# Kernel tuning notes

Measured on AMD Instinct MI355X. Metric: run time of the kernel, lower is better.

Reference implementation:

```python
import jax, jax.numpy as jnp
import numpy as np

B, S, D, H, K = 8, 1024, 512, 512, 8  # batch, seq, input_dim, hidden, max neighbors


def setup_inputs() -> dict:
    key = jax.random.key(0)
    ks = jax.random.split(key, 10)
    p = lambda k, shape: (0.05 * jax.random.normal(k, shape, jnp.float32))
    return {
        "input_t": jax.random.normal(ks[0], (B, S, D), jnp.float32),
        "comb_idx": jax.random.randint(ks[1], (B, S, K), 0, S, jnp.int32),
        "comb_mask": jax.random.randint(ks[2], (B, S, K), 0, 2, jnp.int32),
        "order": jnp.arange(B, dtype=jnp.int64),
        # PyTorch LSTM params per direction; b = b_ih + b_hh fused (mathematically identical)
        "w_ih_f": p(ks[3], (4 * H, D)),
        "w_hh_f": p(ks[4], (4 * H, H)),
        "b_f": p(ks[5], (4 * H,)),
        "w_ih_b": p(ks[6], (4 * H, D)),
        "w_hh_b": p(ks[7], (4 * H, H)),
        "b_b": p(ks[8], (4 * H,)),
    }


def _lstm_scan(x_sbd, w_ih, w_hh, b, reverse):
    # x_sbd: [S, B, D]; PyTorch gate order i, f, g, o; zero initial state (inithidden)
    Bb = x_sbd.shape[1]
    Hh = w_hh.shape[1]
    h0 = jnp.zeros((Bb, Hh), x_sbd.dtype)
    c0 = jnp.zeros((Bb, Hh), x_sbd.dtype)

    def cell(carry, xt):
        h, c = carry
        z = xt @ w_ih.T + h @ w_hh.T + b
        i, f, g, o = jnp.split(z, 4, axis=-1)
        c = jax.nn.sigmoid(f) * c + jax.nn.sigmoid(i) * jnp.tanh(g)
        h = jax.nn.sigmoid(o) * jnp.tanh(c)
        return (h, c), h

    (hn, cn), hs = jax.lax.scan(cell, (h0, c0), x_sbd, reverse=reverse)
    return hs, hn, cn  # hs in original time order even when reverse=True


def reference(input_t, comb_idx, comb_mask, order, w_ih_f, w_hh_f, b_f, w_ih_b, w_hh_b, b_b):
    x = jnp.swapaxes(input_t, 0, 1)  # [S, B, D]
    hs_f, hn_f, cn_f = _lstm_scan(x, w_ih_f, w_hh_f, b_f, reverse=False)
    hs_b, hn_b, cn_b = _lstm_scan(x, w_ih_b, w_hh_b, b_b, reverse=True)
    padded = jnp.swapaxes(jnp.concatenate([hs_f, hs_b], axis=-1), 0, 1)  # [B, S, 2H]
    h_n = jnp.stack([hn_f, hn_b])  # [2, B, H]
    c_n = jnp.stack([cn_f, cn_b])

    # comb = batch_comb[order[idx]]
    ci = comb_idx[order]                                  # [B, S, K]
    cm = comb_mask[order].astype(padded.dtype)            # [B, S, K]
    gathered = jax.vmap(lambda xb, ib: xb[ib])(padded, ci)  # [B, S, K, 2H]
    neigh_sum = (gathered * cm[..., None]).sum(axis=2)    # [B, S, 2H]
    cnt = cm.sum(axis=-1)                                 # [B, S]
    rep = (padded + neigh_sum) / (1.0 + cnt)[..., None]   # (x_i + sum_j x_j) / (|comb_i| + 1)
    rep = rep[:, 1:-1, :]                                 # drop first/last token

    # reorder_batch_encoder_rep[order[i]] = rep[i]
    out = jnp.zeros_like(rep).at[order].set(rep)
    return out, h_n, c_n
```

## Files before the change

kernel.cpp:

```cpp
#include <hip/hip_runtime.h>
#include <stdint.h>

typedef unsigned short u16;
typedef unsigned long long u64;
typedef __attribute__((ext_vector_type(8))) short short8v;
typedef __attribute__((ext_vector_type(4))) float f32x4;

#define OUT_HN   8372224
#define OUT_CN   8380416

#define WS_FLAGS 0
#define WS_CSB   4096
#define WS_HSB0  36864
#define WS_HSB1  8433664
#define WS_ZX    16830464

__device__ __forceinline__ u16 f2bf(float f) {
  uint32_t u = __float_as_uint(f);
  u += 0x7FFFu + ((u >> 16) & 1u);
  return (u16)(u >> 16);
}
__device__ __forceinline__ float bf2f(u16 v) {
  return __uint_as_float(((uint32_t)v) << 16);
}
__device__ __forceinline__ short8v cvt8(const float* p) {
  float4 a = *(const float4*)p;
  float4 b = *(const float4*)(p + 4);
  short8v r;
  r[0] = (short)f2bf(a.x); r[1] = (short)f2bf(a.y);
  r[2] = (short)f2bf(a.z); r[3] = (short)f2bf(a.w);
  r[4] = (short)f2bf(b.x); r[5] = (short)f2bf(b.y);
  r[6] = (short)f2bf(b.z); r[7] = (short)f2bf(b.w);
  return r;
}

__global__ void k_init(uint32_t* flags) {
  if (threadIdx.x < 64) flags[threadIdx.x] = 0;
}

__global__ void k_zero(u16* h0, u16* h1, float* c) {
  int i = blockIdx.x * blockDim.x + threadIdx.x;
  if (i < 4096) { h0[i] = 0; h1[i] = 0; }
  if (i < 8192) c[i] = 0.f;
}

#define STAGE_X(tcol)                                                          \
  {                                                                            \
    _Pragma("unroll")                                                          \
    for (int half = 0; half < 2; ++half) {                                     \
      int g = tid + half * 256;                                                \
      int r = g >> 6, B = g & 63;                                              \
      const float* xr = xf + ((size_t)r * 1024 + (tcol)) * 512 + B * 8;        \
      float4 a = *(const float4*)xr;                                           \
      float4 b = *(const float4*)(xr + 4);                                     \
      short8v v;                                                               \
      v[0] = (short)f2bf(a.x); v[1] = (short)f2bf(a.y);                        \
      v[2] = (short)f2bf(a.z); v[3] = (short)f2bf(a.w);                        \
      v[4] = (short)f2bf(b.x); v[5] = (short)f2bf(b.y);                        \
      v[6] = (short)f2bf(b.z); v[7] = (short)f2bf(b.w);                        \
      *(short8v*)(xL + r * 512 + ((B ^ r) << 3)) = v;                          \
    }                                                                          \
  }

__global__ void k_zx(const float* __restrict__ xf,
                     const float* __restrict__ wihf, const float* __restrict__ wihb,
                     u16* __restrict__ zx, int s0, int seglen)
{
  const int nch  = seglen >> 5;
  const int bid  = blockIdx.x;
  const int chunk = bid % nch;
  const int wg   = (bid / nch) & 15;
  const int dir  = bid / (nch * 16);
  const int tid  = threadIdx.x;
  const int wid  = tid >> 6;
  const int lane = tid & 63;
  const int jbase = wg * 32;
  const float* wih = dir ? wihb : wihf;

  __shared__ u16 xL[8 * 512];
  __shared__ float zL[4 * 8 * 32];

  short8v bih[2][16];
  {
    const int rr = lane & 15;
    const int ko = (lane >> 4) * 8;
    #pragma unroll
    for (int nt = 0; nt < 2; ++nt) {
      const int row = wid * 512 + jbase + nt * 16 + rr;
      #pragma unroll
      for (int kt = 0; kt < 16; ++kt)
        bih[nt][kt] = cvt8(wih + (size_t)row * 512 + kt * 32 + ko);
    }
  }

  const int rB = lane & 7;
  const int q  = lane >> 4;
  const f32x4 fzero = {0.f, 0.f, 0.f, 0.f};

  for (int i = 0; i < 32; ++i) {
    const int sidx = chunk * 32 + i;
    const int gstep = s0 + sidx;
    const int tn = dir ? (1023 - gstep) : gstep;
    STAGE_X(tn);
    __syncthreads();
    f32x4 acc0 = fzero, acc1 = fzero;
    #pragma unroll
    for (int kt = 0; kt < 16; ++kt) {
      short8v ax = *(const short8v*)(xL + rB * 512 + (((kt * 4 + q) ^ rB) << 3));
      acc0 = __builtin_amdgcn_mfma_f32_16x16x32_bf16(ax, bih[0][kt], acc0, 0, 0, 0);
      acc1 = __builtin_amdgcn_mfma_f32_16x16x32_bf16(ax, bih[1][kt], acc1, 0, 0, 0);
    }
    if (lane < 32) {
      #pragma unroll
      for (int r = 0; r < 4; ++r) {
        const int brow = (lane >> 4) * 4 + r;
        zL[wid * 256 + brow * 32 + (lane & 15)]      = acc0[r];
        zL[wid * 256 + brow * 32 + 16 + (lane & 15)] = acc1[r];
      }
    }
    __syncthreads();
    if (tid < 128) {
      const int b = tid >> 4;
      const int r = (tid & 15) * 8;
      const int g = r >> 5;
      const int jj = r & 31;
      short8v v;
      #pragma unroll
      for (int w = 0; w < 8; ++w) v[w] = (short)f2bf(zL[g * 256 + b * 32 + jj + w]);
      *(short8v*)(zx + (((size_t)dir * seglen + sidx) * 16 + wg) * 1024 + tid * 8) = v;
    }
    __syncthreads();
  }
}

__launch_bounds__(256, 1)
__global__ void k_lstm(const float* __restrict__ whhf, const float* __restrict__ whhb,
                       const float* __restrict__ bias0, const float* __restrict__ bias1,
                       const u16* __restrict__ zx,
                       u16* hsb0, u16* hsb1, float* csb, float* out,
                       uint32_t* flags, int s0, int s1, int seglen)
{
  const int tid  = threadIdx.x;
  const int wid  = tid >> 6;
  const int lane = tid & 63;
  const int dir  = blockIdx.x >> 4;
  const int wg   = blockIdx.x & 15;
  const int jbase = wg * 32;

  const float* whh  = dir ? whhb : whhf;
  const float* bias = dir ? bias1 : bias0;
  u16* hsb = dir ? hsb1 : hsb0;
  uint32_t* fl = flags + dir * 16;

  __shared__ u16 hL[8 * 512];
  __shared__ float zL[4 * 8 * 32];
  __shared__ u16 hS[8 * 32];
  __shared__ u64 zxL[256];

  short8v bhh[2][16];
  {
    const int rr = lane & 15;
    const int ko = (lane >> 4) * 8;
    #pragma unroll
    for (int nt = 0; nt < 2; ++nt) {
      const int row = wid * 512 + jbase + nt * 16 + rr;
      #pragma unroll
      for (int kt = 0; kt < 16; ++kt)
        bhh[nt][kt] = cvt8(whh + (size_t)row * 512 + kt * 32 + ko);
    }
  }

  const int cb = tid >> 5;
  const int cj = tid & 31;
  const float bz0 = bias[0 * 512 + jbase + cj];
  const float bz1 = bias[1 * 512 + jbase + cj];
  const float bz2 = bias[2 * 512 + jbase + cj];
  const float bz3 = bias[3 * 512 + jbase + cj];
  float* cp = csb + dir * 4096 + cb * 512 + jbase + cj;
  float c_state = *cp;

  const int rB = lane & 7;
  const int q  = lane >> 4;
  const f32x4 fzero = {0.f, 0.f, 0.f, 0.f};
  const u16* zx16 = (const u16*)zxL;

  for (int gstep = s0; gstep < s1; ++gstep) {
    {
      const u64* zp = (const u64*)(zx + (((size_t)dir * seglen + (gstep - s0)) * 16 + wg) * 1024);
      zxL[tid] = zp[tid];
    }
    if (tid < 16) {
      int guard = 0;
      while (__hip_atomic_load(&fl[tid], __ATOMIC_RELAXED, __HIP_MEMORY_SCOPE_AGENT)
             < (uint32_t)gstep && ++guard < (1 << 15)) { }
    }
    __syncthreads();
    {
      const u16* base = hsb + (size_t)gstep * 4096 + tid * 16;
      short8v v0, v1;
      asm volatile("global_load_dwordx4 %0, %1, off sc1"
                   : "=v"(v0) : "v"(base));
      asm volatile("global_load_dwordx4 %0, %1, off offset:16 sc1"
                   : "=v"(v1) : "v"(base));
      asm volatile("s_waitcnt vmcnt(0)" ::: "memory");
      int G0 = 2 * tid, G1 = 2 * tid + 1;
      int r0 = G0 >> 6, B0 = G0 & 63;
      int r1 = G1 >> 6, B1 = G1 & 63;
      *(short8v*)(hL + r0 * 512 + ((B0 ^ r0) << 3)) = v0;
      *(short8v*)(hL + r1 * 512 + ((B1 ^ r1) << 3)) = v1;
    }
    __syncthreads();
    f32x4 acc0 = fzero, acc1 = fzero;
    #pragma unroll
    for (int kt = 0; kt < 16; ++kt) {
      short8v ah = *(const short8v*)(hL + rB * 512 + (((kt * 4 + q) ^ rB) << 3));
      acc0 = __builtin_amdgcn_mfma_f32_16x16x32_bf16(ah, bhh[0][kt], acc0, 0, 0, 0);
      acc1 = __builtin_amdgcn_mfma_f32_16x16x32_bf16(ah, bhh[1][kt], acc1, 0, 0, 0);
    }
    if (lane < 32) {
      #pragma unroll
      for (int r = 0; r < 4; ++r) {
        const int brow = (lane >> 4) * 4 + r;
        zL[wid * 256 + brow * 32 + (lane & 15)]      = acc0[r];
        zL[wid * 256 + brow * 32 + 16 + (lane & 15)] = acc1[r];
      }
    }
    __syncthreads();
    {
      float zi = zL[0 * 256 + cb * 32 + cj] + bz0 + bf2f(zx16[cb * 128 +  0 + cj]);
      float zf = zL[1 * 256 + cb * 32 + cj] + bz1 + bf2f(zx16[cb * 128 + 32 + cj]);
      float zg = zL[2 * 256 + cb * 32 + cj] + bz2 + bf2f(zx16[cb * 128 + 64 + cj]);
      float zo = zL[3 * 256 + cb * 32 + cj] + bz3 + bf2f(zx16[cb * 128 + 96 + cj]);
      float si = 1.f / (1.f + __expf(-zi));
      float sf = 1.f / (1.f + __expf(-zf));
      float so = 1.f / (1.f + __expf(-zo));
      float ag = fabsf(zg); float eg = __expf(-2.f * ag);
      float tg = (1.f - eg) / (1.f + eg); tg = copysignf(tg, zg);
      c_state = sf * c_state + si * tg;
      float ac = fabsf(c_state); float ec = __expf(-2.f * ac);
      float tc = (1.f - ec) / (1.f + ec); tc = copysignf(tc, c_state);
      float h = so * tc;
      hS[cb * 32 + cj] = f2bf(h);
      if (gstep == 1023) {
        out[OUT_HN + dir * 4096 + cb * 512 + jbase + cj] = h;
        out[OUT_CN + dir * 4096 + cb * 512 + jbase + cj] = c_state;
      }
    }
    __syncthreads();
    if (tid < 32) {
      const int pb = tid >> 2;
      const int pt = tid & 3;
      short8v hv = *(const short8v*)(hS + pb * 32 + 8 * pt);
      u16* dst = hsb + ((size_t)(gstep + 1) * 8 + pb) * 512 + jbase + 8 * pt;
      asm volatile("global_store_dwordx4 %0, %1, off sc1"
                   :: "v"(dst), "v"(hv) : "memory");
      asm volatile("s_waitcnt vmcnt(0)" ::: "memory");
    }
    if (tid == 0) {
      __hip_atomic_store(&fl[wg], (uint32_t)(gstep + 1), __ATOMIC_RELAXED,
                         __HIP_MEMORY_SCOPE_AGENT);
    }
  }
  *cp = c_state;
}

__global__ void k_combine(const u16* __restrict__ hsb0, const u16* __restrict__ hsb1,
                          const int* __restrict__ cidx, const int* __restrict__ cmask,
                          const int* __restrict__ order, float* __restrict__ out)
{
  const int tid = threadIdx.x;
  const int b = blockIdx.x / 1022;
  const int s = 1 + (blockIdx.x % 1022);
  __shared__ int sidx[8];
  __shared__ float smask[8];
  __shared__ int rsh;
  if (tid == 0) rsh = order[b];
  __syncthreads();
  const int r = rsh;
  if (tid < 8) {
    size_t base = ((size_t)r * 1024 + s) * 8 + tid;
    sidx[tid] = cidx[base];
    smask[tid] = (float)cmask[base];
  }
  __syncthreads();
  float cnt = 0.f;
  #pragma unroll
  for (int k = 0; k < 8; ++k) cnt += smask[k];
  const float inv = 1.f / (1.f + cnt);

  const int col0 = tid * 4;
  const bool isF = col0 < 512;
  const int cloc = isF ? col0 : col0 - 512;
  const u16* hb = isF ? hsb0 : hsb1;

  float v0, v1, v2, v3;
  {
    size_t ci2 = isF ? (size_t)(s + 1) : (size_t)(1024 - s);
    ushort4 qv = *(const ushort4*)(hb + (ci2 * 8 + b) * 512 + cloc);
    v0 = bf2f(qv.x); v1 = bf2f(qv.y); v2 = bf2f(qv.z); v3 = bf2f(qv.w);
  }
  #pragma unroll
  for (int k = 0; k < 8; ++k) {
    float m = smask[k];
    if (m != 0.f) {
      int sp = sidx[k];
      size_t ci2 = isF ? (size_t)(sp + 1) : (size_t)(1024 - sp);
      ushort4 qv = *(const ushort4*)(hb + (ci2 * 8 + b) * 512 + cloc);
      v0 += m * bf2f(qv.x); v1 += m * bf2f(qv.y); v2 += m * bf2f(qv.z); v3 += m * bf2f(qv.w);
    }
  }
  size_t ob = ((size_t)r * 1022 + (s - 1)) * 1024 + col0;
  float4 ov; ov.x = v0 * inv; ov.y = v1 * inv; ov.z = v2 * inv; ov.w = v3 * inv;
  *(float4*)(out + ob) = ov;
}

extern "C" void kernel_launch(void* const* d_in, const int* in_sizes, int n_in,
                              void* d_out, int out_size, void* d_ws, size_t ws_size,
                              hipStream_t stream)
{
  const float* x      = (const float*)d_in[0];
  const int*   cidx   = (const int*)d_in[1];
  const int*   cmask  = (const int*)d_in[2];
  const int*   order  = (const int*)d_in[3];
  const float* wihf = (const float*)d_in[4];
  const float* whhf = (const float*)d_in[5];
  const float* bf   = (const float*)d_in[6];
  const float* wihb = (const float*)d_in[7];
  const float* whhb = (const float*)d_in[8];
  const float* bb   = (const float*)d_in[9];
  float* out = (float*)d_out;

  char* ws = (char*)d_ws;
  uint32_t* FLAGS = (uint32_t*)(ws + WS_FLAGS);
  float* CSB = (float*)(ws + WS_CSB);
  u16* HSB0 = (u16*)(ws + WS_HSB0);
  u16* HSB1 = (u16*)(ws + WS_HSB1);
  u16* ZX   = (u16*)(ws + WS_ZX);

  const int seglen = (ws_size >= (size_t)WS_ZX + 1024ull * 65536) ? 1024 : 128;

  hipLaunchKernelGGL(k_init, dim3(1), dim3(64), 0, stream, FLAGS);
  hipLaunchKernelGGL(k_zero, dim3(32), dim3(256), 0, stream, HSB0, HSB1, CSB);

  for (int s0 = 0; s0 < 1024; s0 += seglen) {
    hipLaunchKernelGGL(k_zx, dim3(2 * 16 * (seglen >> 5)), dim3(256), 0, stream,
                       x, wihf, wihb, ZX, s0, seglen);
    hipLaunchKernelGGL(k_lstm, dim3(32), dim3(256), 0, stream,
                       whhf, whhb, bf, bb, ZX, HSB0, HSB1, CSB, out, FLAGS,
                       s0, s0 + seglen, seglen);
  }

  hipLaunchKernelGGL(k_combine, dim3(8 * 1022), dim3(256), 0, stream,
                     HSB0, HSB1, cidx, cmask, order, out);
}
```

Measured before the change: 2.961 ms.

## Interleave forward and backward LSTM directions within each workgroup

The recurrent kernel now launches 16 workgroups instead of 32. Each workgroup holds both directions' W_hh slices in registers and runs a forward step and then a backward step in every loop iteration. The aim is to halve the number of workgroups taking part in cross-workgroup flag synchronisation, and to let one direction's spin-wait overlap with the other direction's compute. The cost is that each workgroup does twice the serial work per step and needs twice the weight registers, which risks spills. With the serialised phases, the per-step latency could grow.

```diff
diff --git a/kernel.cpp b/kernel.cpp
--- a/kernel.cpp
+++ b/kernel.cpp
@@ -133,6 +133,86 @@
   }
 }
 
+#define PHASE(D, BHH, BZ, CS)                                                  \
+  {                                                                            \
+    u16* hsb_ = (D) ? hsb1 : hsb0;                                             \
+    uint32_t* fl_ = flags + (D) * 16;                                          \
+    {                                                                          \
+      const u64* zp = (const u64*)(zx + (((size_t)(D) * seglen + (gstep - s0)) * 16 + wg) * 1024); \
+      zxL[tid] = zp[tid];                                                      \
+    }                                                                          \
+    if (tid < 16) {                                                            \
+      int guard = 0;                                                           \
+      while (__hip_atomic_load(&fl_[tid], __ATOMIC_RELAXED, __HIP_MEMORY_SCOPE_AGENT) \
+             < (uint32_t)gstep && ++guard < (1 << 15)) { }                     \
+    }                                                                          \
+    __syncthreads();                           \
+    {                                                                          \
+      const u16* base = hsb_ + (size_t)gstep * 4096 + tid * 16;                \
+      short8v v0, v1;                                                          \
+      asm volatile("global_load_dwordx4 %0, %1, off sc1" : "=v"(v0) : "v"(base)); \
+      asm volatile("global_load_dwordx4 %0, %1, off offset:16 sc1" : "=v"(v1) : "v"(base)); \
+      asm volatile("s_waitcnt vmcnt(0)" ::: "memory");                         \
+      int G0 = 2 * tid, G1 = 2 * tid + 1;                                      \
+      int r0 = G0 >> 6, B0 = G0 & 63;                                          \
+      int r1 = G1 >> 6, B1 = G1 & 63;                                          \
+      *(short8v*)(hL + r0 * 512 + ((B0 ^ r0) << 3)) = v0;                      \
+      *(short8v*)(hL + r1 * 512 + ((B1 ^ r1) << 3)) = v1;                      \
+    }                                                                          \
+    __syncthreads();                                                    \
+    {                                                                          \
+      f32x4 acc0 = fzero, acc1 = fzero;                                        \
+      _Pragma("unroll")                                                        \
+      for (int kt = 0; kt < 16; ++kt) {                                        \
+        short8v ah = *(const short8v*)(hL + rB * 512 + (((kt * 4 + q) ^ rB) << 3)); \
+        acc0 = __builtin_amdgcn_mfma_f32_16x16x32_bf16(ah, BHH[0][kt], acc0, 0, 0, 0); \
+        acc1 = __builtin_amdgcn_mfma_f32_16x16x32_bf16(ah, BHH[1][kt], acc1, 0, 0, 0); \
+      }                                                                        \
+      if (lane < 32) {                                                         \
+        _Pragma("unroll")                                                      \
+        for (int r = 0; r < 4; ++r) {                                          \
+          const int brow = (lane >> 4) * 4 + r;                                \
+          zL[wid * 256 + brow * 32 + (lane & 15)]      = acc0[r];              \
+          zL[wid * 256 + brow * 32 + 16 + (lane & 15)] = acc1[r];              \
+        }                                                                      \
+      }                                                                        \
+    }                                                                          \
+    __syncthreads();                                                    \
+    {                                                                          \
+      float zi = zL[0 * 256 + cb * 32 + cj] + BZ[0] + bf2f(zx16[cb * 128 +  0 + cj]); \
+      float zf = zL[1 * 256 + cb * 32 + cj] + BZ[1] + bf2f(zx16[cb * 128 + 32 + cj]); \
+      float zg = zL[2 * 256 + cb * 32 + cj] + BZ[2] + bf2f(zx16[cb * 128 + 64 + cj]); \
+      float zo = zL[3 * 256 + cb * 32 + cj] + BZ[3] + bf2f(zx16[cb * 128 + 96 + cj]); \
+      float si = 1.f / (1.f + __expf(-zi));                                    \
+      float sf = 1.f / (1.f + __expf(-zf));                                    \
+      float so = 1.f / (1.f + __expf(-zo));                                    \
+      float ag = fabsf(zg); float eg = __expf(-2.f * ag);                      \
+      float tg = (1.f - eg) / (1.f + eg); tg = copysignf(tg, zg);              \
+      CS = sf * CS + si * tg;                                                  \
+      float ac = fabsf(CS); float ec = __expf(-2.f * ac);                      \
+      float tc = (1.f - ec) / (1.f + ec); tc = copysignf(tc, CS);              \
+      float h = so * tc;                                                       \
+      hS[cb * 32 + cj] = f2bf(h);                                              \
+      if (gstep == 1023) {                                                     \
+        out[OUT_HN + (D) * 4096 + cb * 512 + jbase + cj] = h;                  \
+        out[OUT_CN + (D) * 4096 + cb * 512 + jbase + cj] = CS;                 \
+      }                                                                        \
+    }                                                                          \
+    __syncthreads();                                       \
+    if (tid < 32) {                                                            \
+      const int pb = tid >> 2;                                                 \
+      const int pt = tid & 3;                                                  \
+      short8v hv = *(const short8v*)(hS + pb * 32 + 8 * pt);                   \
+      u16* dst = hsb_ + ((size_t)(gstep + 1) * 8 + pb) * 512 + jbase + 8 * pt; \
+      asm volatile("global_store_dwordx4 %0, %1, off sc1" :: "v"(dst), "v"(hv) : "memory"); \
+      asm volatile("s_waitcnt vmcnt(0)" ::: "memory");                         \
+    }                                                                          \
+    if (tid == 0) {                                                            \
+      __hip_atomic_store(&fl_[wg], (uint32_t)(gstep + 1), __ATOMIC_RELAXED,    \
+                         __HIP_MEMORY_SCOPE_AGENT);                            \
+    }                                                                          \
+  }
+
 __launch_bounds__(256, 1)
 __global__ void k_lstm(const float* __restrict__ whhf, const float* __restrict__ whhb,
                        const float* __restrict__ bias0, const float* __restrict__ bias1,
@@ -143,21 +223,15 @@
   const int tid  = threadIdx.x;
   const int wid  = tid >> 6;
   const int lane = tid & 63;
-  const int dir  = blockIdx.x >> 4;
-  const int wg   = blockIdx.x & 15;
+  const int wg   = blockIdx.x;
   const int jbase = wg * 32;
-
-  const float* whh  = dir ? whhb : whhf;
-  const float* bias = dir ? bias1 : bias0;
-  u16* hsb = dir ? hsb1 : hsb0;
-  uint32_t* fl = flags + dir * 16;
 
   __shared__ u16 hL[8 * 512];
   __shared__ float zL[4 * 8 * 32];
   __shared__ u16 hS[8 * 32];
   __shared__ u64 zxL[256];
 
-  short8v bhh[2][16];
+  short8v bhhF[2][16], bhhB[2][16];
   {
     const int rr = lane & 15;
     const int ko = (lane >> 4) * 8;
@@ -165,19 +239,25 @@
     for (int nt = 0; nt < 2; ++nt) {
       const int row = wid * 512 + jbase + nt * 16 + rr;
       #pragma unroll
-      for (int kt = 0; kt < 16; ++kt)
-        bhh[nt][kt] = cvt8(whh + (size_t)row * 512 + kt * 32 + ko);
+      for (int kt = 0; kt < 16; ++kt) {
+        bhhF[nt][kt] = cvt8(whhf + (size_t)row * 512 + kt * 32 + ko);
+        bhhB[nt][kt] = cvt8(whhb + (size_t)row * 512 + kt * 32 + ko);
+      }
     }
   }
 
   const int cb = tid >> 5;
   const int cj = tid & 31;
-  const float bz0 = bias[0 * 512 + jbase + cj];
-  const float bz1 = bias[1 * 512 + jbase + cj];
-  const float bz2 = bias[2 * 512 + jbase + cj];
-  const float bz3 = bias[3 * 512 + jbase + cj];
-  float* cp = csb + dir * 4096 + cb * 512 + jbase + cj;
-  float c_state = *cp;
+  float bzF[4], bzB[4];
+  #pragma unroll
+  for (int g = 0; g < 4; ++g) {
+    bzF[g] = bias0[g * 512 + jbase + cj];
+    bzB[g] = bias1[g * 512 + jbase + cj];
+  }
+  float* cpF = csb + 0 * 4096 + cb * 512 + jbase + cj;
+  float* cpB = csb + 1 * 4096 + cb * 512 + jbase + cj;
+  float c_f = *cpF;
+  float c_b = *cpB;
 
   const int rB = lane & 7;
   const int q  = lane >> 4;
@@ -185,83 +265,11 @@
   const u16* zx16 = (const u16*)zxL;
 
   for (int gstep = s0; gstep < s1; ++gstep) {
-    {
-      const u64* zp = (const u64*)(zx + (((size_t)dir * seglen + (gstep - s0)) * 16 + wg) * 1024);
-      zxL[tid] = zp[tid];
-    }
-    if (tid < 16) {
-      int guard = 0;
-      while (__hip_atomic_load(&fl[tid], __ATOMIC_RELAXED, __HIP_MEMORY_SCOPE_AGENT)
-             < (uint32_t)gstep && ++guard < (1 << 15)) { }
-    }
-    __syncthreads();
-    {
-      const u16* base = hsb + (size_t)gstep * 4096 + tid * 16;
-      short8v v0, v1;
-      asm volatile("global_load_dwordx4 %0, %1, off sc1"
-                   : "=v"(v0) : "v"(base));
-      asm volatile("global_load_dwordx4 %0, %1, off offset:16 sc1"
-                   : "=v"(v1) : "v"(base));
-      asm volatile("s_waitcnt vmcnt(0)" ::: "memory");
-      int G0 = 2 * tid, G1 = 2 * tid + 1;
-      int r0 = G0 >> 6, B0 = G0 & 63;
-      int r1 = G1 >> 6, B1 = G1 & 63;
-      *(short8v*)(hL + r0 * 512 + ((B0 ^ r0) << 3)) = v0;
-      *(short8v*)(hL + r1 * 512 + ((B1 ^ r1) << 3)) = v1;
-    }
-    __syncthreads();
-    f32x4 acc0 = fzero, acc1 = fzero;
-    #pragma unroll
-    for (int kt = 0; kt < 16; ++kt) {
-      short8v ah = *(const short8v*)(hL + rB * 512 + (((kt * 4 + q) ^ rB) << 3));
-      acc0 = __builtin_amdgcn_mfma_f32_16x16x32_bf16(ah, bhh[0][kt], acc0, 0, 0, 0);
-      acc1 = __builtin_amdgcn_mfma_f32_16x16x32_bf16(ah, bhh[1][kt], acc1, 0, 0, 0);
-    }
-    if (lane < 32) {
-      #pragma unroll
-      for (int r = 0; r < 4; ++r) {
-        const int brow = (lane >> 4) * 4 + r;
-        zL[wid * 256 + brow * 32 + (lane & 15)]      = acc0[r];
-        zL[wid * 256 + brow * 32 + 16 + (lane & 15)] = acc1[r];
-      }
-    }
-    __syncthreads();
-    {
-      float zi = zL[0 * 256 + cb * 32 + cj] + bz0 + bf2f(zx16[cb * 128 +  0 + cj]);
-      float zf = zL[1 * 256 + cb * 32 + cj] + bz1 + bf2f(zx16[cb * 128 + 32 + cj]);
-      float zg = zL[2 * 256 + cb * 32 + cj] + bz2 + bf2f(zx16[cb * 128 + 64 + cj]);
-      float zo = zL[3 * 256 + cb * 32 + cj] + bz3 + bf2f(zx16[cb * 128 + 96 + cj]);
-      float si = 1.f / (1.f + __expf(-zi));
-      float sf = 1.f / (1.f + __expf(-zf));
-      float so = 1.f / (1.f + __expf(-zo));
-      float ag = fabsf(zg); float eg = __expf(-2.f * ag);
-      float tg = (1.f - eg) / (1.f + eg); tg = copysignf(tg, zg);
-      c_state = sf * c_state + si * tg;
-      float ac = fabsf(c_state); float ec = __expf(-2.f * ac);
-      float tc = (1.f - ec) / (1.f + ec); tc = copysignf(tc, c_state);
-      float h = so * tc;
-      hS[cb * 32 + cj] = f2bf(h);
-      if (gstep == 1023) {
-        out[OUT_HN + dir * 4096 + cb * 512 + jbase + cj] = h;
-        out[OUT_CN + dir * 4096 + cb * 512 + jbase + cj] = c_state;
-      }
-    }
-    __syncthreads();
-    if (tid < 32) {
-      const int pb = tid >> 2;
-      const int pt = tid & 3;
-      short8v hv = *(const short8v*)(hS + pb * 32 + 8 * pt);
-      u16* dst = hsb + ((size_t)(gstep + 1) * 8 + pb) * 512 + jbase + 8 * pt;
-      asm volatile("global_store_dwordx4 %0, %1, off sc1"
-                   :: "v"(dst), "v"(hv) : "memory");
-      asm volatile("s_waitcnt vmcnt(0)" ::: "memory");
-    }
-    if (tid == 0) {
-      __hip_atomic_store(&fl[wg], (uint32_t)(gstep + 1), __ATOMIC_RELAXED,
-                         __HIP_MEMORY_SCOPE_AGENT);
-    }
-  }
-  *cp = c_state;
+    PHASE(0, bhhF, bzF, c_f)
+    PHASE(1, bhhB, bzB, c_b)
+  }
+  *cpF = c_f;
+  *cpB = c_b;
 }
 
 __global__ void k_combine(const u16* __restrict__ hsb0, const u16* __restrict__ hsb1,
@@ -345,7 +353,7 @@
   for (int s0 = 0; s0 < 1024; s0 += seglen) {
     hipLaunchKernelGGL(k_zx, dim3(2 * 16 * (seglen >> 5)), dim3(256), 0, stream,
                        x, wihf, wihb, ZX, s0, seglen);
-    hipLaunchKernelGGL(k_lstm, dim3(32), dim3(256), 0, stream,
+    hipLaunchKernelGGL(k_lstm, dim3(16), dim3(256), 0, stream,
                        whhf, whhb, bf, bb, ZX, HSB0, HSB1, CSB, out, FLAGS,
                        s0, s0 + seglen, seglen);
   }
```

New measurement: 5.477 ms. 1.85x slower.
